# Performance work log

Measured on AMD Instinct MI355X. Metric: run time of the kernel, lower is better.

Reference implementation:

```python
import jax, jax.numpy as jnp
import numpy as np

A_PARAM = 1.4   # double-well parameter 'a' (non-trainable)
DT = 0.1        # Euler step


def setup_inputs() -> dict:
    key = jax.random.key(0)
    B, N, K, TMAX = 16384, 256, 10, 64
    k0, k1, k2, k3 = jax.random.split(key, 4)
    x = jax.random.normal(k0, (B, N), jnp.float32)
    # trainable base: orthogonal columns, gain 1.15 (Orthogonal initializer)
    m = jax.random.normal(k1, (N, N - K), jnp.float32)
    q, _ = jnp.linalg.qr(m)
    base_train = (1.15 * q).astype(jnp.float32)
    # fixed base = attractor vectors (rec_base)
    base_fix = jax.random.normal(k2, (N, K), jnp.float32)
    # trainable eigenvalues ~ N(-5, 1)
    autov_tr = (-5.0 + jax.random.normal(k3, (N - K,), jnp.float32))
    gamma = jnp.asarray(0.2, jnp.float32)
    return {"x": x, "base_train": base_train, "base_fix": base_fix,
            "autov_tr": autov_tr, "gamma": gamma, "tmax": TMAX}


def reference(x, base_train, base_fix, autov_tr, gamma, tmax):
    N = x.shape[1]
    a, dt = A_PARAM, DT
    beta = np.float32(1.0 / np.sqrt(N))
    # eigenvalues: trainable then fixed zeros (attractor eigenvalues)
    eig = jnp.concatenate([autov_tr, jnp.zeros(base_fix.shape[1], x.dtype)])
    x_max = 8.0 * a ** 2 * gamma * np.float32(np.sqrt(N)) - 0.1
    eig = jnp.clip(eig, -1e9, x_max)
    base = jnp.concatenate([base_train, base_fix], axis=1)   # [N, N]
    # A = base @ diag(eig) @ inv(base)  (constant across all Euler steps)
    A = (base * eig[None, :]) @ jnp.linalg.inv(base)
    lim = 10.0 * a
    gabs = jnp.abs(gamma)

    def step(xc, _):
        dw = 4.0 * gabs * (xc * (a ** 2) - xc ** 3)          # double-well dynamics
        xn = xc + dt * (dw + (xc @ A.T) * beta)
        return jnp.clip(xn, -lim, lim), None

    xf, _ = jax.lax.scan(step, x, None, length=tmax)
    return xf
```

## Files before the change

kernel.cpp:

```cpp
#include <hip/hip_runtime.h>
#include <hip/hip_bf16.h>

#define NDIM 256
#define NKD  246
#define KD   10
#define TMAXS 64
#define APAR 1.4f
#define DTS  0.1f

typedef _Float16 f16x8 __attribute__((ext_vector_type(8)));
typedef float    f32x4 __attribute__((ext_vector_type(4)));

__global__ void k_prep(const float* __restrict__ bt, const float* __restrict__ bf,
                       const float* __restrict__ autov, const float* __restrict__ gamma,
                       float* __restrict__ base, float* __restrict__ eig) {
  int r = blockIdx.x, c = threadIdx.x;
  float v = (c < NKD) ? bt[r*NKD + c] : bf[r*KD + (c - NKD)];
  base[r*NDIM + c] = v;
  if (r == 0) {
    float g = gamma[0];
    float xmax = 8.0f*APAR*APAR*g*16.0f - 0.1f;
    float e = (c < NKD) ? autov[c] : 0.0f;
    e = fminf(e, xmax);
    e = fmaxf(e, -1e9f);
    eig[c] = e;
  }
}

__global__ void k_stgR(const float* __restrict__ base, double* __restrict__ StG,
                       double* __restrict__ Rm) {
  __shared__ double sg[NKD];
  const int j = blockIdx.x, t = threadIdx.x;
  if (t < NKD) {
    double acc = 0.0;
    for (int r = 0; r < NDIM; ++r)
      acc += (double)base[r*NDIM + t] * (double)base[r*NDIM + NKD + j];
    sg[t] = acc;
    StG[t*KD + j] = acc;
  }
  __syncthreads();
  double acc = 0.0;
  for (int i = 0; i < NKD; ++i)
    acc += (double)base[t*NDIM + i] * sg[i];
  Rm[t*KD + j] = (double)base[t*NDIM + NKD + j] - acc * (1.0/1.3225);
}

__global__ void k_m10x2(const float* __restrict__ base, const double* __restrict__ Rm,
                        double* __restrict__ X) {
  __shared__ double M[KD][2*KD];
  __shared__ double fcol[KD];
  __shared__ int piv;
  const int t = threadIdx.x;
  if (t < KD*KD) {
    int j1 = t / KD, j2 = t % KD;
    double acc = 0.0;
    for (int r = 0; r < NDIM; ++r)
      acc += Rm[r*KD + j1] * (double)base[r*NDIM + NKD + j2];
    M[j1][j2] = acc;
    M[j1][KD + j2] = (j1 == j2) ? 1.0 : 0.0;
  }
  __syncthreads();
  for (int k = 0; k < KD; ++k) {
    if (t == 0) {
      int p = k; double mv = fabs(M[k][k]);
      for (int r = k + 1; r < KD; ++r) { double v = fabs(M[r][k]); if (v > mv) { mv = v; p = r; } }
      piv = p;
    }
    __syncthreads();
    int p = piv;
    if (p != k && t < 2*KD) { double tmp = M[k][t]; M[k][t] = M[p][t]; M[p][t] = tmp; }
    __syncthreads();
    double pv = M[k][k];
    __syncthreads();
    if (t < 2*KD) M[k][t] /= pv;
    if (t < KD) fcol[t] = M[t][k];
    __syncthreads();
    if (t < KD*2*KD) {
      int r = t / (2*KD), c = t % (2*KD);
      if (r != k) M[r][c] -= fcol[r] * M[k][c];
    }
    __syncthreads();
  }
  for (int j = 0; j < KD; ++j) {
    double acc = 0.0;
    for (int l = 0; l < KD; ++l) acc += M[j][KD + l] * Rm[t*KD + l];
    X[(NKD + j)*NDIM + t] = acc;
  }
}

__global__ void k_x1(const float* __restrict__ base, const double* __restrict__ StG,
                     double* __restrict__ X) {
  int c = blockIdx.x, i = threadIdx.x;
  if (i >= NKD) return;
  double acc = 0.0;
  for (int j = 0; j < KD; ++j) acc += StG[i*KD + j] * X[(NKD + j)*NDIM + c];
  X[i*NDIM + c] = ((double)base[c*NDIM + i] - acc) * (1.0/1.3225);
}

__global__ void k_T(const float* __restrict__ base, const double* __restrict__ X,
                    double* __restrict__ T) {
  int i = blockIdx.x, j = threadIdx.x;
  double acc = 0.0;
  for (int k = 0; k < NDIM; ++k) acc += (double)base[i*NDIM + k] * X[k*NDIM + j];
  T[i*NDIM + j] = ((i == j) ? 2.0 : 0.0) - acc;
}
__global__ void k_XT(const double* __restrict__ X, const double* __restrict__ T,
                     double* __restrict__ Xo) {
  int i = blockIdx.x, j = threadIdx.x;
  double acc = 0.0;
  for (int k = 0; k < NDIM; ++k) acc += X[i*NDIM + k] * T[k*NDIM + j];
  Xo[i*NDIM + j] = acc;
}

__global__ void k_Atpack(const float* __restrict__ base, const float* __restrict__ eig,
                         const double* __restrict__ X, _Float16* __restrict__ Bh,
                         _Float16* __restrict__ Bl) {
  int j = blockIdx.x;
  int k = threadIdx.x;
  double acc = 0.0;
  for (int m = 0; m < NDIM; ++m)
    acc += (double)base[j*NDIM + m] * (double)eig[m] * X[m*NDIM + k];
  float v = (float)acc;
  _Float16 h  = (_Float16)v;
  _Float16 lo = (_Float16)(v - (float)h);
  int kc = k >> 5, g = (k >> 3) & 3, jj = k & 7;
  int idx = (((kc*4 + g)*NDIM + j) << 3) + jj;
  Bh[idx] = h; Bl[idx] = lo;
}

__global__ __launch_bounds__(512, 2)
void k_evolve(const float* __restrict__ x_in, const f16x8* __restrict__ Bh,
              const f16x8* __restrict__ Bl, const float* __restrict__ gamma,
              float* __restrict__ out) {
  __shared__ float xsT[NDIM][68];
  __shared__ f16x8 xhp[4][8][4][16];
  __shared__ f16x8 xlp[4][8][4][16];

  const int t  = threadIdx.x;
  const int w  = t >> 6;
  const int l  = t & 63;
  const int lg = l >> 4;
  const int lr = l & 15;
  const int rbase = blockIdx.x * 64;

  const float g   = fabsf(gamma[0]);
  const float c4g = 4.0f * g;
  const float a2  = APAR * APAR;
  const float lim = 10.0f * APAR;
  const float dtb = DTS * 0.0625f;

  float xr[4][2][4];
  #pragma unroll
  for (int mt = 0; mt < 4; ++mt)
    #pragma unroll
    for (int nt = 0; nt < 2; ++nt) {
      const int col = w*32 + nt*16 + lr;
      #pragma unroll
      for (int r = 0; r < 4; ++r)
        xr[mt][nt][r] = x_in[(rbase + mt*16 + lg*4 + r)*NDIM + col];
    }

  f16x8 bhf[2][8], blf[2][8];
  #pragma unroll
  for (int nt = 0; nt < 2; ++nt) {
    const int col = w*32 + nt*16 + lr;
    #pragma unroll
    for (int kc = 0; kc < 8; ++kc) {
      bhf[nt][kc] = Bh[(kc*4 + lg)*NDIM + col];
      blf[nt][kc] = Bl[(kc*4 + lg)*NDIM + col];
    }
  }

  auto writeXS = [&]() {
    #pragma unroll
    for (int mt = 0; mt < 4; ++mt)
      #pragma unroll
      for (int nt = 0; nt < 2; ++nt) {
        const int col = w*32 + nt*16 + lr;
        f32x4 v = { xr[mt][nt][0], xr[mt][nt][1], xr[mt][nt][2], xr[mt][nt][3] };
        *(f32x4*)&xsT[col][mt*16 + lg*4] = v;
      }
  };
  auto convert = [&]() {
    #pragma unroll
    for (int i = 0; i < 4; ++i) {
      const int idx = t + i*512;
      const int row = idx & 63;
      const int kcg = idx >> 6;
      const int kc = kcg >> 2, gg = kcg & 3;
      float vv[8];
      #pragma unroll
      for (int j = 0; j < 8; ++j) vv[j] = xsT[kc*32 + gg*8 + j][row];
      f16x8 h, lo;
      #pragma unroll
      for (int j = 0; j < 4; ++j) {
        auto hp = __builtin_amdgcn_cvt_pkrtz(vv[2*j], vv[2*j+1]);
        h[2*j]   = (_Float16)hp[0];
        h[2*j+1] = (_Float16)hp[1];
        float r0 = vv[2*j]   - (float)hp[0];
        float r1 = vv[2*j+1] - (float)hp[1];
        auto lp = __builtin_amdgcn_cvt_pkrtz(r0, r1);
        lo[2*j]   = (_Float16)lp[0];
        lo[2*j+1] = (_Float16)lp[1];
      }
      xhp[row >> 4][kc][gg][row & 15] = h;
      xlp[row >> 4][kc][gg][row & 15] = lo;
    }
  };

  writeXS();
  __syncthreads();
  convert();
  __syncthreads();

  for (int step = 0; step < TMAXS; ++step) {
    f32x4 acc[4][2] = {};
    #pragma unroll
    for (int kc = 0; kc < 8; ++kc) {
      #pragma unroll
      for (int mt = 0; mt < 4; ++mt) {
        f16x8 ah = xhp[mt][kc][lg][lr];
        f16x8 al = xlp[mt][kc][lg][lr];
        #pragma unroll
        for (int nt = 0; nt < 2; ++nt) {
          acc[mt][nt] = __builtin_amdgcn_mfma_f32_16x16x32_f16(ah, bhf[nt][kc], acc[mt][nt], 0, 0, 0);
          acc[mt][nt] = __builtin_amdgcn_mfma_f32_16x16x32_f16(ah, blf[nt][kc], acc[mt][nt], 0, 0, 0);
          acc[mt][nt] = __builtin_amdgcn_mfma_f32_16x16x32_f16(al, bhf[nt][kc], acc[mt][nt], 0, 0, 0);
        }
      }
    }
    #pragma unroll
    for (int mt = 0; mt < 4; ++mt)
      #pragma unroll
      for (int nt = 0; nt < 2; ++nt)
        #pragma unroll
        for (int r = 0; r < 4; ++r) {
          float xc = xr[mt][nt][r];
          float xn = xc + DTS*(c4g*(a2*xc - xc*xc*xc)) + dtb*acc[mt][nt][r];
          xn = fminf(fmaxf(xn, -lim), lim);
          xr[mt][nt][r] = xn;
        }
    writeXS();
    __syncthreads();
    convert();
    __syncthreads();
  }

  #pragma unroll
  for (int mt = 0; mt < 4; ++mt)
    #pragma unroll
    for (int nt = 0; nt < 2; ++nt) {
      const int col = w*32 + nt*16 + lr;
      #pragma unroll
      for (int r = 0; r < 4; ++r)
        out[(rbase + mt*16 + lg*4 + r)*NDIM + col] = xr[mt][nt][r];
    }
}

extern "C" void kernel_launch(void* const* d_in, const int* in_sizes, int n_in,
                              void* d_out, int out_size, void* d_ws, size_t ws_size,
                              hipStream_t stream) {
  const float* x  = (const float*)d_in[0];
  const float* bt = (const float*)d_in[1];
  const float* bf = (const float*)d_in[2];
  const float* av = (const float*)d_in[3];
  const float* gm = (const float*)d_in[4];
  float* out = (float*)d_out;
  const int Brows = in_sizes[0] / NDIM;

  float*  base = (float*)d_ws;
  float*  eig  = base + NDIM*NDIM;
  double* Xd   = (double*)(eig + NDIM);
  double* Xe   = Xd + NDIM*NDIM;
  double* Td   = Xe + NDIM*NDIM;
  double* StG  = Td + NDIM*NDIM;
  double* Rm   = StG + 2560;
  _Float16* Bph = (_Float16*)(Rm + 2560);
  _Float16* Bpl = Bph + NDIM*NDIM;

  k_prep <<<NDIM, NDIM, 0, stream>>>(bt, bf, av, gm, base, eig);
  k_stgR <<<KD,   NDIM, 0, stream>>>(base, StG, Rm);
  k_m10x2<<<1,    NDIM, 0, stream>>>(base, Rm, Xd);
  k_x1   <<<NDIM, NDIM, 0, stream>>>(base, StG, Xd);
  k_T <<<NDIM, NDIM, 0, stream>>>(base, Xd, Td);
  k_XT<<<NDIM, NDIM, 0, stream>>>(Xd, Td, Xe);

  k_Atpack<<<NDIM, NDIM, 0, stream>>>(base, eig, Xe, Bph, Bpl);

  k_evolve<<<Brows/64, 512, 0, stream>>>(x, (const f16x8*)Bph, (const f16x8*)Bpl, gm, out);
}
```

Baseline: 443.3 us.

## Swap MFMA operand roles and double-buffer state to drop transpose pass

The kernel now computes the transposed product, with A held in registers as the row operand and the state vector as the column operand. The MFMA output layout then matches the next step's input layout, so each lane can convert and write its own results directly to shared memory. This removes the fp32 transpose buffer and one barrier per step. The shared fragment buffers are double-buffered so a single sync per step suffices, and global loads and stores become 16-byte vector accesses.

After: 420.0 us. 5.2% less time.

```diff
diff --git a/kernel.cpp b/kernel.cpp
--- a/kernel.cpp
+++ b/kernel.cpp
@@ -112,29 +112,28 @@
   Xo[i*NDIM + j] = acc;
 }
 
-__global__ void k_Atpack(const float* __restrict__ base, const float* __restrict__ eig,
-                         const double* __restrict__ X, _Float16* __restrict__ Bh,
-                         _Float16* __restrict__ Bl) {
-  int j = blockIdx.x;
+__global__ void k_Afrag(const float* __restrict__ base, const float* __restrict__ eig,
+                        const double* __restrict__ X, _Float16* __restrict__ Ah,
+                        _Float16* __restrict__ Al) {
+  int m = blockIdx.x;
   int k = threadIdx.x;
   double acc = 0.0;
-  for (int m = 0; m < NDIM; ++m)
-    acc += (double)base[j*NDIM + m] * (double)eig[m] * X[m*NDIM + k];
+  for (int q = 0; q < NDIM; ++q)
+    acc += (double)base[m*NDIM + q] * (double)eig[q] * X[q*NDIM + k];
   float v = (float)acc;
   _Float16 h  = (_Float16)v;
   _Float16 lo = (_Float16)(v - (float)h);
-  int kc = k >> 5, g = (k >> 3) & 3, jj = k & 7;
-  int idx = (((kc*4 + g)*NDIM + j) << 3) + jj;
-  Bh[idx] = h; Bl[idx] = lo;
+  int kc = k >> 5, lg = (k >> 3) & 3, jj = k & 7;
+  int idx = (((kc*NDIM + m)*4 + lg) << 3) + jj;
+  Ah[idx] = h; Al[idx] = lo;
 }
 
 __global__ __launch_bounds__(512, 2)
-void k_evolve(const float* __restrict__ x_in, const f16x8* __restrict__ Bh,
-              const f16x8* __restrict__ Bl, const float* __restrict__ gamma,
+void k_evolve(const float* __restrict__ x_in, const f16x8* __restrict__ Ah,
+              const f16x8* __restrict__ Al, const float* __restrict__ gamma,
               float* __restrict__ out) {
-  __shared__ float xsT[NDIM][68];
-  __shared__ f16x8 xhp[4][8][4][16];
-  __shared__ f16x8 xlp[4][8][4][16];
+  __shared__ f16x8 zh[2][8][4][64];
+  __shared__ f16x8 zl[2][8][4][64];
 
   const int t  = threadIdx.x;
   const int w  = t >> 6;
@@ -149,90 +148,83 @@
   const float lim = 10.0f * APAR;
   const float dtb = DTS * 0.0625f;
 
-  float xr[4][2][4];
+  f16x8 ahf[2][8], alf[2][8];
   #pragma unroll
-  for (int mt = 0; mt < 4; ++mt)
-    #pragma unroll
-    for (int nt = 0; nt < 2; ++nt) {
-      const int col = w*32 + nt*16 + lr;
-      #pragma unroll
-      for (int r = 0; r < 4; ++r)
-        xr[mt][nt][r] = x_in[(rbase + mt*16 + lg*4 + r)*NDIM + col];
-    }
-
-  f16x8 bhf[2][8], blf[2][8];
+  for (int mt = 0; mt < 2; ++mt) {
+    const int m = w*32 + mt*16 + lr;
+    #pragma unroll
+    for (int kc = 0; kc < 8; ++kc) {
+      ahf[mt][kc] = Ah[(kc*NDIM + m)*4 + lg];
+      alf[mt][kc] = Al[(kc*NDIM + m)*4 + lg];
+    }
+  }
+
+  f32x4 xr[2][4];
   #pragma unroll
-  for (int nt = 0; nt < 2; ++nt) {
-    const int col = w*32 + nt*16 + lr;
+  for (int mt = 0; mt < 2; ++mt)
+    #pragma unroll
+    for (int nt = 0; nt < 4; ++nt) {
+      const int row = rbase + nt*16 + lr;
+      const int col = w*32 + mt*16 + lg*4;
+      xr[mt][nt] = *(const f32x4*)&x_in[row*NDIM + col];
+    }
+
+  const int lp   = (lg >> 1)*16 + lr;
+  const int boff = (lg & 1)*8;
+
+  auto emit = [&](int b) {
+    #pragma unroll
+    for (int mt = 0; mt < 2; ++mt) {
+      const int tl = mt*32 + lp;
+      #pragma unroll
+      for (int nt = 0; nt < 4; ++nt) {
+        f32x4 v = xr[mt][nt];
+        auto h01 = __builtin_amdgcn_cvt_pkrtz(v[0], v[1]);
+        auto h23 = __builtin_amdgcn_cvt_pkrtz(v[2], v[3]);
+        float r0 = v[0] - (float)h01[0];
+        float r1 = v[1] - (float)h01[1];
+        float r2 = v[2] - (float)h23[0];
+        float r3 = v[3] - (float)h23[1];
+        auto l01 = __builtin_amdgcn_cvt_pkrtz(r0, r1);
+        auto l23 = __builtin_amdgcn_cvt_pkrtz(r2, r3);
+        uint2 uh, ul;
+        __builtin_memcpy(&uh.x, &h01, 4);
+        __builtin_memcpy(&uh.y, &h23, 4);
+        __builtin_memcpy(&ul.x, &l01, 4);
+        __builtin_memcpy(&ul.y, &l23, 4);
+        *(uint2*)((char*)&zh[b][w][nt][tl] + boff) = uh;
+        *(uint2*)((char*)&zl[b][w][nt][tl] + boff) = ul;
+      }
+    }
+  };
+
+  emit(0);
+  __syncthreads();
+
+  for (int step = 0; step < TMAXS; ++step) {
+    const int rb = step & 1, wb = rb ^ 1;
+    f32x4 acc[2][4] = {};
     #pragma unroll
     for (int kc = 0; kc < 8; ++kc) {
-      bhf[nt][kc] = Bh[(kc*4 + lg)*NDIM + col];
-      blf[nt][kc] = Bl[(kc*4 + lg)*NDIM + col];
-    }
-  }
-
-  auto writeXS = [&]() {
-    #pragma unroll
-    for (int mt = 0; mt < 4; ++mt)
-      #pragma unroll
-      for (int nt = 0; nt < 2; ++nt) {
-        const int col = w*32 + nt*16 + lr;
-        f32x4 v = { xr[mt][nt][0], xr[mt][nt][1], xr[mt][nt][2], xr[mt][nt][3] };
-        *(f32x4*)&xsT[col][mt*16 + lg*4] = v;
+      f16x8 bh[4], bl[4];
+      #pragma unroll
+      for (int nt = 0; nt < 4; ++nt) {
+        bh[nt] = zh[rb][kc][nt][l];
+        bl[nt] = zl[rb][kc][nt][l];
       }
-  };
-  auto convert = [&]() {
-    #pragma unroll
-    for (int i = 0; i < 4; ++i) {
-      const int idx = t + i*512;
-      const int row = idx & 63;
-      const int kcg = idx >> 6;
-      const int kc = kcg >> 2, gg = kcg & 3;
-      float vv[8];
-      #pragma unroll
-      for (int j = 0; j < 8; ++j) vv[j] = xsT[kc*32 + gg*8 + j][row];
-      f16x8 h, lo;
-      #pragma unroll
-      for (int j = 0; j < 4; ++j) {
-        auto hp = __builtin_amdgcn_cvt_pkrtz(vv[2*j], vv[2*j+1]);
-        h[2*j]   = (_Float16)hp[0];
-        h[2*j+1] = (_Float16)hp[1];
-        float r0 = vv[2*j]   - (float)hp[0];
-        float r1 = vv[2*j+1] - (float)hp[1];
-        auto lp = __builtin_amdgcn_cvt_pkrtz(r0, r1);
-        lo[2*j]   = (_Float16)lp[0];
-        lo[2*j+1] = (_Float16)lp[1];
-      }
-      xhp[row >> 4][kc][gg][row & 15] = h;
-      xlp[row >> 4][kc][gg][row & 15] = lo;
-    }
-  };
-
-  writeXS();
-  __syncthreads();
-  convert();
-  __syncthreads();
-
-  for (int step = 0; step < TMAXS; ++step) {
-    f32x4 acc[4][2] = {};
-    #pragma unroll
-    for (int kc = 0; kc < 8; ++kc) {
-      #pragma unroll
-      for (int mt = 0; mt < 4; ++mt) {
-        f16x8 ah = xhp[mt][kc][lg][lr];
-        f16x8 al = xlp[mt][kc][lg][lr];
+      #pragma unroll
+      for (int mt = 0; mt < 2; ++mt)
         #pragma unroll
-        for (int nt = 0; nt < 2; ++nt) {
-          acc[mt][nt] = __builtin_amdgcn_mfma_f32_16x16x32_f16(ah, bhf[nt][kc], acc[mt][nt], 0, 0, 0);
-          acc[mt][nt] = __builtin_amdgcn_mfma_f32_16x16x32_f16(ah, blf[nt][kc], acc[mt][nt], 0, 0, 0);
-          acc[mt][nt] = __builtin_amdgcn_mfma_f32_16x16x32_f16(al, bhf[nt][kc], acc[mt][nt], 0, 0, 0);
+        for (int nt = 0; nt < 4; ++nt) {
+          acc[mt][nt] = __builtin_amdgcn_mfma_f32_16x16x32_f16(ahf[mt][kc], bh[nt], acc[mt][nt], 0, 0, 0);
+          acc[mt][nt] = __builtin_amdgcn_mfma_f32_16x16x32_f16(ahf[mt][kc], bl[nt], acc[mt][nt], 0, 0, 0);
+          acc[mt][nt] = __builtin_amdgcn_mfma_f32_16x16x32_f16(alf[mt][kc], bh[nt], acc[mt][nt], 0, 0, 0);
         }
-      }
-    }
-    #pragma unroll
-    for (int mt = 0; mt < 4; ++mt)
-      #pragma unroll
-      for (int nt = 0; nt < 2; ++nt)
+    }
+    #pragma unroll
+    for (int mt = 0; mt < 2; ++mt)
+      #pragma unroll
+      for (int nt = 0; nt < 4; ++nt)
         #pragma unroll
         for (int r = 0; r < 4; ++r) {
           float xc = xr[mt][nt][r];
@@ -240,20 +232,17 @@
           xn = fminf(fmaxf(xn, -lim), lim);
           xr[mt][nt][r] = xn;
         }
-    writeXS();
-    __syncthreads();
-    convert();
+    emit(wb);
     __syncthreads();
   }
 
   #pragma unroll
-  for (int mt = 0; mt < 4; ++mt)
-    #pragma unroll
-    for (int nt = 0; nt < 2; ++nt) {
-      const int col = w*32 + nt*16 + lr;
-      #pragma unroll
-      for (int r = 0; r < 4; ++r)
-        out[(rbase + mt*16 + lg*4 + r)*NDIM + col] = xr[mt][nt][r];
+  for (int mt = 0; mt < 2; ++mt)
+    #pragma unroll
+    for (int nt = 0; nt < 4; ++nt) {
+      const int row = rbase + nt*16 + lr;
+      const int col = w*32 + mt*16 + lg*4;
+      *(f32x4*)&out[row*NDIM + col] = xr[mt][nt];
     }
 }
 
@@ -275,8 +264,8 @@
   double* Td   = Xe + NDIM*NDIM;
   double* StG  = Td + NDIM*NDIM;
   double* Rm   = StG + 2560;
-  _Float16* Bph = (_Float16*)(Rm + 2560);
-  _Float16* Bpl = Bph + NDIM*NDIM;
+  _Float16* Aph = (_Float16*)(Rm + 2560);
+  _Float16* Apl = Aph + NDIM*NDIM;
 
   k_prep <<<NDIM, NDIM, 0, stream>>>(bt, bf, av, gm, base, eig);
   k_stgR <<<KD,   NDIM, 0, stream>>>(base, StG, Rm);
@@ -285,7 +274,7 @@
   k_T <<<NDIM, NDIM, 0, stream>>>(base, Xd, Td);
   k_XT<<<NDIM, NDIM, 0, stream>>>(Xd, Td, Xe);
 
-  k_Atpack<<<NDIM, NDIM, 0, stream>>>(base, eig, Xe, Bph, Bpl);
-
-  k_evolve<<<Brows/64, 512, 0, stream>>>(x, (const f16x8*)Bph, (const f16x8*)Bpl, gm, out);
-}
+  k_Afrag<<<NDIM, NDIM, 0, stream>>>(base, eig, Xe, Aph, Apl);
+
+  k_evolve<<<Brows/64, 512, 0, stream>>>(x, (const f16x8*)Aph, (const f16x8*)Apl, gm, out);
+}
```
